# Kernel tuning notes

Hardware: AMD Instinct MI355X
Metric: run time of the kernel (lower is better)

## Reference

```python
import jax, jax.numpy as jnp
import numpy as np

B, L = 2048, 4096


def setup_inputs() -> dict:
    key = jax.random.key(0)
    k1, k2, k3 = jax.random.split(key, 3)
    j = jax.random.normal(k1, (1,), dtype=jnp.float32)
    b = jax.random.normal(k2, (2,), dtype=jnp.float32)
    observations = jax.random.randint(k3, (B, L), 0, 2, dtype=jnp.int64)
    return {"j": j, "b": b, "observations": observations}


def reference(j, b, observations):
    dt = j.dtype
    values = jnp.array([-0.5, 0.5], dtype=dt)           # 2 latent states
    pairs = values[:, None] * values[None, :]            # [2,2] outer product
    psi = j * pairs                                      # pairwise max-plus potential [2,2]
    # unary potentials: phi[b_idx, i, s] = b[obs[b_idx, i]] * values[s]
    phi = b[observations][..., None] * values            # [B, L, 2]
    zeros2 = jnp.zeros((2,), dtype=dt)

    def step(msg, phi_i):
        # max-plus message update: max over source state s of phi[s] + psi[s,t] + msg[s]
        new = jnp.max(phi_i[:, None] + psi + msg[:, None], axis=0)
        return new, new

    def per_seq(phi_seq):  # phi_seq: [L, 2]
        # forward messages: column 0 is zeros, column i+1 is msg from step i (i = 0..L-2)
        _, f = jax.lax.scan(step, zeros2, phi_seq[:-1])
        fwd = jnp.concatenate([zeros2[None], f], axis=0)       # [L, 2]
        # backward messages: iterate i = L-1 down to 1; msg from step i lands at column i-1
        _, bk = jax.lax.scan(step, zeros2, phi_seq[:0:-1])
        bwd = jnp.concatenate([bk[::-1], zeros2[None]], axis=0)  # [L, 2]
        return (phi_seq + fwd + bwd).T                          # [2, L]

    return jax.vmap(per_seq)(phi)  # [B, 2, L]
```

## Files before the change

### kernel.cpp

```cpp
#include <hip/hip_runtime.h>
#include <math.h>

#define L_SEQ 4096
#define NT 512
#define CHUNK 8
#define NW (NT/64)

struct M2 { float a00, a01, a10, a11; };

__device__ __forceinline__ M2 mpc(const M2& A, const M2& B) {
  M2 C;
  C.a00 = fmaxf(A.a00 + B.a00, A.a01 + B.a10);
  C.a01 = fmaxf(A.a00 + B.a01, A.a01 + B.a11);
  C.a10 = fmaxf(A.a10 + B.a00, A.a11 + B.a10);
  C.a11 = fmaxf(A.a10 + B.a01, A.a11 + B.a11);
  return C;
}

__device__ __forceinline__ M2 ldm(const float4& v) { return M2{v.x, v.y, v.z, v.w}; }
__device__ __forceinline__ float4 stm(const M2& m) { return make_float4(m.a00, m.a01, m.a10, m.a11); }

template <int CTRL>
__device__ __forceinline__ float dppf(float x) {
  return __int_as_float(__builtin_amdgcn_update_dpp(
      0, __float_as_int(x), CTRL, 0xf, 0xf, true));
}
template <int CTRL>
__device__ __forceinline__ M2 dpp_fetch(const M2& x) {
  M2 r;
  r.a00 = dppf<CTRL>(x.a00); r.a01 = dppf<CTRL>(x.a01);
  r.a10 = dppf<CTRL>(x.a10); r.a11 = dppf<CTRL>(x.a11);
  return r;
}

__global__ __launch_bounds__(NT, 8) void chain_fb_kernel(
    const float* __restrict__ jp, const float* __restrict__ bp,
    const int* __restrict__ obs, float* __restrict__ out) {
  __shared__ float4 T4s[16];
  __shared__ float T8a[256], T8b[256], T8c[256], T8d[256];
  __shared__ float4 wtf[NW];
  __shared__ float4 wtb[NW];

  const int t = threadIdx.x;
  const int lane = t & 63;
  const int w = t >> 6;
  const long b = blockIdx.x;

  const float P   = 0.25f * jp[0];
  const float hb0 = 0.5f * bp[0];
  const float hb1 = 0.5f * bp[1];

  const int4* rowp = (const int4*)(obs + b * L_SEQ + (long)t * CHUNK);
  int4 q0 = rowp[0], q1 = rowp[1];

  if (t < 16) {
    float u0 = (t & 1) ? hb1 : hb0;
    M2 Tt{P - u0, -u0 - P, u0 - P, u0 + P};
    #pragma unroll
    for (int k = 1; k < 4; ++k) {
      float uk = ((t >> k) & 1) ? hb1 : hb0;
      M2 Ek{P - uk, -uk - P, uk - P, uk + P};
      Tt = mpc(Tt, Ek);
    }
    T4s[t] = stm(Tt);
  }
  __syncthreads();
  if (t < 256) {
    M2 M = mpc(ldm(T4s[t & 15]), ldm(T4s[(t >> 4) & 15]));
    T8a[t] = M.a00; T8b[t] = M.a01; T8c[t] = M.a10; T8d[t] = M.a11;
  }
  const unsigned m =
      (unsigned)(q0.x & 1)       | (unsigned)(q0.y & 1) << 1 |
      (unsigned)(q0.z & 1) << 2  | (unsigned)(q0.w & 1) << 3 |
      (unsigned)(q1.x & 1) << 4  | (unsigned)(q1.y & 1) << 5 |
      (unsigned)(q1.z & 1) << 6  | (unsigned)(q1.w & 1) << 7;
  __syncthreads();

  const unsigned mrev = (unsigned)__shfl((int)m, 63 - lane);
  const unsigned r = __brev(mrev) >> 24;
  M2 T {T8a[m], T8b[m], T8c[m], T8d[m]};
  M2 Rv{T8a[r], T8b[r], T8c[r], T8d[r]};

  {
    M2 f, g;
    f = dpp_fetch<0x111>(T); g = dpp_fetch<0x111>(Rv);
    if ((lane & 15) >= 1) { T = mpc(f, T); Rv = mpc(g, Rv); }
    f = dpp_fetch<0x112>(T); g = dpp_fetch<0x112>(Rv);
    if ((lane & 15) >= 2) { T = mpc(f, T); Rv = mpc(g, Rv); }
    f = dpp_fetch<0x114>(T); g = dpp_fetch<0x114>(Rv);
    if ((lane & 15) >= 4) { T = mpc(f, T); Rv = mpc(g, Rv); }
    f = dpp_fetch<0x118>(T); g = dpp_fetch<0x118>(Rv);
    if ((lane & 15) >= 8) { T = mpc(f, T); Rv = mpc(g, Rv); }
    f = dpp_fetch<0x142>(T); g = dpp_fetch<0x142>(Rv);
    if (lane & 16)        { T = mpc(f, T); Rv = mpc(g, Rv); }
    f = dpp_fetch<0x143>(T); g = dpp_fetch<0x143>(Rv);
    if (lane >= 32)       { T = mpc(f, T); Rv = mpc(g, Rv); }
  }
  if (lane == 63) { wtf[w] = stm(T); wtb[w] = stm(Rv); }

  M2 EF{__shfl_up(T.a00, 1), __shfl_up(T.a01, 1),
        __shfl_up(T.a10, 1), __shfl_up(T.a11, 1)};
  M2 EB{__shfl_up(Rv.a00, 1), __shfl_up(Rv.a01, 1),
        __shfl_up(Rv.a10, 1), __shfl_up(Rv.a11, 1)};
  if (lane == 0) {
    EF.a00 = 0.f; EF.a01 = -INFINITY; EF.a10 = -INFINITY; EF.a11 = 0.f;
    EB.a00 = 0.f; EB.a01 = -INFINITY; EB.a10 = -INFINITY; EB.a11 = 0.f;
  }

  __syncthreads();

  M2 GF = EF, GB = EB;
  for (int ww = w - 1; ww >= 0; --ww) GF = mpc(ldm(wtf[ww]), GF);
  for (int ww = w + 1; ww < NW; ++ww) GB = mpc(ldm(wtb[ww]), GB);
  float fm0 = fmaxf(GF.a00, GF.a10), fm1 = fmaxf(GF.a01, GF.a11);
  const float bv0 = fmaxf(GB.a00, GB.a10), bv1 = fmaxf(GB.a01, GB.a11);
  float bm0 = __shfl(bv0, 63 - lane);
  float bm1 = __shfl(bv1, 63 - lane);

  float o0[CHUNK], o1[CHUNK];
  #pragma unroll
  for (int e = 0; e < CHUNK; ++e) {
    float u = ((m >> e) & 1) ? hb1 : hb0;
    float x = fm0 - u, y = fm1 + u;
    o0[e] = x; o1[e] = y;
    fm0 = fmaxf(x + P, y - P);
    fm1 = fmaxf(x - P, y + P);
  }
  #pragma unroll
  for (int e = CHUNK - 1; e >= 0; --e) {
    float u = ((m >> e) & 1) ? hb1 : hb0;
    o0[e] += bm0; o1[e] += bm1;
    float x = bm0 - u, y = bm1 + u;
    bm0 = fmaxf(x + P, y - P);
    bm1 = fmaxf(x - P, y + P);
  }

  const long base = (long)t * CHUNK;
  float* r0 = out + b * (2L * L_SEQ) + base;
  float* r1 = r0 + L_SEQ;
  ((float4*)r0)[0] = make_float4(o0[0], o0[1], o0[2], o0[3]);
  ((float4*)r0)[1] = make_float4(o0[4], o0[5], o0[6], o0[7]);
  ((float4*)r1)[0] = make_float4(o1[0], o1[1], o1[2], o1[3]);
  ((float4*)r1)[1] = make_float4(o1[4], o1[5], o1[6], o1[7]);
}

extern "C" void kernel_launch(void* const* d_in, const int* in_sizes, int n_in,
                              void* d_out, int out_size, void* d_ws, size_t ws_size,
                              hipStream_t stream) {
  const float* jp  = (const float*)d_in[0];
  const float* bp  = (const float*)d_in[1];
  const int*   obs = (const int*)d_in[2];
  float* out = (float*)d_out;
  const int B = in_sizes[2] / L_SEQ;
  chain_fb_kernel<<<B, NT, 0, stream>>>(jp, bp, obs, out);
}
```

Baseline: 24.61 us.

## Split chain scan into segment-totals and output kernels via workspace

Replaces the single 512-thread-per-sequence kernel with two launches. The first computes per-wave segment transfer matrices into a global workspace. The second recomputes the local scan, combines prefix and suffix segment totals read from global memory, and writes the outputs. This removes block-wide syncs on the combine and makes the blocks smaller, but it reads observations twice, repeats the LUT build and scan, and adds a second launch.

After: 32.47 us. 1.32x slower.

```diff
diff --git a/kernel.cpp b/kernel.cpp
--- a/kernel.cpp
+++ b/kernel.cpp
@@ -2,9 +2,10 @@
 #include <math.h>
 
 #define L_SEQ 4096
-#define NT 512
+#define SEG 512
+#define NSEG 8
+#define NT 256
 #define CHUNK 8
-#define NW (NT/64)
 
 struct M2 { float a00, a01, a10, a11; };
 
@@ -33,26 +34,9 @@
   return r;
 }
 
-__global__ __launch_bounds__(NT, 8) void chain_fb_kernel(
-    const float* __restrict__ jp, const float* __restrict__ bp,
-    const int* __restrict__ obs, float* __restrict__ out) {
-  __shared__ float4 T4s[16];
-  __shared__ float T8a[256], T8b[256], T8c[256], T8d[256];
-  __shared__ float4 wtf[NW];
-  __shared__ float4 wtb[NW];
-
-  const int t = threadIdx.x;
-  const int lane = t & 63;
-  const int w = t >> 6;
-  const long b = blockIdx.x;
-
-  const float P   = 0.25f * jp[0];
-  const float hb0 = 0.5f * bp[0];
-  const float hb1 = 0.5f * bp[1];
-
-  const int4* rowp = (const int4*)(obs + b * L_SEQ + (long)t * CHUNK);
-  int4 q0 = rowp[0], q1 = rowp[1];
-
+__device__ __forceinline__ void build_lut(
+    int t, float P, float hb0, float hb1, float4* T4s,
+    float* T8a, float* T8b, float* T8c, float* T8d) {
   if (t < 16) {
     float u0 = (t & 1) ? hb1 : hb0;
     M2 Tt{P - u0, -u0 - P, u0 - P, u0 + P};
@@ -65,38 +49,99 @@
     T4s[t] = stm(Tt);
   }
   __syncthreads();
-  if (t < 256) {
+  {
     M2 M = mpc(ldm(T4s[t & 15]), ldm(T4s[(t >> 4) & 15]));
     T8a[t] = M.a00; T8b[t] = M.a01; T8c[t] = M.a10; T8d[t] = M.a11;
   }
+  __syncthreads();
+}
+
+__device__ __forceinline__ void dpp_dual_scan(M2& T, M2& Rv, int lane) {
+  M2 f, g;
+  f = dpp_fetch<0x111>(T); g = dpp_fetch<0x111>(Rv);
+  if ((lane & 15) >= 1) { T = mpc(f, T); Rv = mpc(g, Rv); }
+  f = dpp_fetch<0x112>(T); g = dpp_fetch<0x112>(Rv);
+  if ((lane & 15) >= 2) { T = mpc(f, T); Rv = mpc(g, Rv); }
+  f = dpp_fetch<0x114>(T); g = dpp_fetch<0x114>(Rv);
+  if ((lane & 15) >= 4) { T = mpc(f, T); Rv = mpc(g, Rv); }
+  f = dpp_fetch<0x118>(T); g = dpp_fetch<0x118>(Rv);
+  if ((lane & 15) >= 8) { T = mpc(f, T); Rv = mpc(g, Rv); }
+  f = dpp_fetch<0x142>(T); g = dpp_fetch<0x142>(Rv);
+  if (lane & 16)        { T = mpc(f, T); Rv = mpc(g, Rv); }
+  f = dpp_fetch<0x143>(T); g = dpp_fetch<0x143>(Rv);
+  if (lane >= 32)       { T = mpc(f, T); Rv = mpc(g, Rv); }
+}
+
+__global__ __launch_bounds__(NT, 8) void seg_totals_kernel(
+    const float* __restrict__ jp, const float* __restrict__ bp,
+    const int* __restrict__ obs, float4* __restrict__ ws) {
+  __shared__ float4 T4s[16];
+  __shared__ float T8a[256], T8b[256], T8c[256], T8d[256];
+
+  const int t = threadIdx.x;
+  const int lane = t & 63;
+  const long g = (long)blockIdx.x * (NT / 64) + (t >> 6);
+
+  const float P   = 0.25f * jp[0];
+  const float hb0 = 0.5f * bp[0];
+  const float hb1 = 0.5f * bp[1];
+
+  const int4* rowp = (const int4*)(obs + g * SEG + lane * CHUNK);
+  int4 q0 = rowp[0], q1 = rowp[1];
+
+  build_lut(t, P, hb0, hb1, T4s, T8a, T8b, T8c, T8d);
+
   const unsigned m =
       (unsigned)(q0.x & 1)       | (unsigned)(q0.y & 1) << 1 |
       (unsigned)(q0.z & 1) << 2  | (unsigned)(q0.w & 1) << 3 |
       (unsigned)(q1.x & 1) << 4  | (unsigned)(q1.y & 1) << 5 |
       (unsigned)(q1.z & 1) << 6  | (unsigned)(q1.w & 1) << 7;
-  __syncthreads();
-
   const unsigned mrev = (unsigned)__shfl((int)m, 63 - lane);
   const unsigned r = __brev(mrev) >> 24;
   M2 T {T8a[m], T8b[m], T8c[m], T8d[m]};
   M2 Rv{T8a[r], T8b[r], T8c[r], T8d[r]};
 
-  {
-    M2 f, g;
-    f = dpp_fetch<0x111>(T); g = dpp_fetch<0x111>(Rv);
-    if ((lane & 15) >= 1) { T = mpc(f, T); Rv = mpc(g, Rv); }
-    f = dpp_fetch<0x112>(T); g = dpp_fetch<0x112>(Rv);
-    if ((lane & 15) >= 2) { T = mpc(f, T); Rv = mpc(g, Rv); }
-    f = dpp_fetch<0x114>(T); g = dpp_fetch<0x114>(Rv);
-    if ((lane & 15) >= 4) { T = mpc(f, T); Rv = mpc(g, Rv); }
-    f = dpp_fetch<0x118>(T); g = dpp_fetch<0x118>(Rv);
-    if ((lane & 15) >= 8) { T = mpc(f, T); Rv = mpc(g, Rv); }
-    f = dpp_fetch<0x142>(T); g = dpp_fetch<0x142>(Rv);
-    if (lane & 16)        { T = mpc(f, T); Rv = mpc(g, Rv); }
-    f = dpp_fetch<0x143>(T); g = dpp_fetch<0x143>(Rv);
-    if (lane >= 32)       { T = mpc(f, T); Rv = mpc(g, Rv); }
-  }
-  if (lane == 63) { wtf[w] = stm(T); wtb[w] = stm(Rv); }
+  dpp_dual_scan(T, Rv, lane);
+
+  if (lane == 63) {
+    ws[2 * g]     = stm(T);
+    ws[2 * g + 1] = stm(Rv);
+  }
+}
+
+__global__ __launch_bounds__(NT, 8) void chain_out_kernel(
+    const float* __restrict__ jp, const float* __restrict__ bp,
+    const int* __restrict__ obs, const float4* __restrict__ ws,
+    float* __restrict__ out) {
+  __shared__ float4 T4s[16];
+  __shared__ float T8a[256], T8b[256], T8c[256], T8d[256];
+
+  const int t = threadIdx.x;
+  const int lane = t & 63;
+  const long g = (long)blockIdx.x * (NT / 64) + (t >> 6);
+  const long seq = g >> 3;
+  const int  seg = (int)(g & 7);
+
+  const float P   = 0.25f * jp[0];
+  const float hb0 = 0.5f * bp[0];
+  const float hb1 = 0.5f * bp[1];
+
+  const int4* rowp = (const int4*)(obs + g * SEG + lane * CHUNK);
+  int4 q0 = rowp[0], q1 = rowp[1];
+
+  build_lut(t, P, hb0, hb1, T4s, T8a, T8b, T8c, T8d);
+
+  const unsigned m =
+      (unsigned)(q0.x & 1)       | (unsigned)(q0.y & 1) << 1 |
+      (unsigned)(q0.z & 1) << 2  | (unsigned)(q0.w & 1) << 3 |
+      (unsigned)(q1.x & 1) << 4  | (unsigned)(q1.y & 1) << 5 |
+      (unsigned)(q1.z & 1) << 6  | (unsigned)(q1.w & 1) << 7;
+  const unsigned mrev = (unsigned)__shfl((int)m, 63 - lane);
+  const unsigned r = __brev(mrev) >> 24;
+  M2 T {T8a[m], T8b[m], T8c[m], T8d[m]};
+  M2 Rv{T8a[r], T8b[r], T8c[r], T8d[r]};
+
+  dpp_dual_scan(T, Rv, lane);
 
   M2 EF{__shfl_up(T.a00, 1), __shfl_up(T.a01, 1),
         __shfl_up(T.a10, 1), __shfl_up(T.a11, 1)};
@@ -107,11 +152,10 @@
     EB.a00 = 0.f; EB.a01 = -INFINITY; EB.a10 = -INFINITY; EB.a11 = 0.f;
   }
 
-  __syncthreads();
-
   M2 GF = EF, GB = EB;
-  for (int ww = w - 1; ww >= 0; --ww) GF = mpc(ldm(wtf[ww]), GF);
-  for (int ww = w + 1; ww < NW; ++ww) GB = mpc(ldm(wtb[ww]), GB);
+  for (int s = seg - 1; s >= 0; --s) GF = mpc(ldm(ws[2 * (seq * NSEG + s)]), GF);
+  for (int s = seg + 1; s < NSEG; ++s) GB = mpc(ldm(ws[2 * (seq * NSEG + s) + 1]), GB);
+
   float fm0 = fmaxf(GF.a00, GF.a10), fm1 = fmaxf(GF.a01, GF.a11);
   const float bv0 = fmaxf(GB.a00, GB.a10), bv1 = fmaxf(GB.a01, GB.a11);
   float bm0 = __shfl(bv0, 63 - lane);
@@ -135,8 +179,8 @@
     bm1 = fmaxf(x - P, y + P);
   }
 
-  const long base = (long)t * CHUNK;
-  float* r0 = out + b * (2L * L_SEQ) + base;
+  const long base = (long)seg * SEG + lane * CHUNK;
+  float* r0 = out + seq * (2L * L_SEQ) + base;
   float* r1 = r0 + L_SEQ;
   ((float4*)r0)[0] = make_float4(o0[0], o0[1], o0[2], o0[3]);
   ((float4*)r0)[1] = make_float4(o0[4], o0[5], o0[6], o0[7]);
@@ -151,6 +195,10 @@
   const float* bp  = (const float*)d_in[1];
   const int*   obs = (const int*)d_in[2];
   float* out = (float*)d_out;
+  float4* ws = (float4*)d_ws;
   const int B = in_sizes[2] / L_SEQ;
-  chain_fb_kernel<<<B, NT, 0, stream>>>(jp, bp, obs, out);
-}
+  const int nseg_total = B * NSEG;
+  const int blocks = nseg_total / (NT / 64);
+  seg_totals_kernel<<<blocks, NT, 0, stream>>>(jp, bp, obs, ws);
+  chain_out_kernel<<<blocks, NT, 0, stream>>>(jp, bp, obs, ws, out);
+}
```

## Packed float2 max-plus math and DPP-based cross-wave prefix with vector-matrix apply

Applied to the files above, without the earlier changes.

Stores the 2x2 max-plus matrices as float2 rows so the additions can map to packed fp32 instructions on CDNA. It replaces the serial per-wave loop over earlier wave totals with a small DPP scan over the 8 wave aggregates, read out with readlane. Each lane now applies the incoming vector to its own inclusive prefix and takes the exclusive value from its neighbour through a DPP shift, where it used to carry full matrices and use shfl_up. The aim is to cut ALU and shuffle work in a latency-bound kernel, with some extra DPP steps and more subtle boundary logic as the cost.

After: 23.21 us. 5.7% less time.

```diff
diff --git a/kernel.cpp b/kernel.cpp
--- a/kernel.cpp
+++ b/kernel.cpp
@@ -6,19 +6,27 @@
 #define CHUNK 8
 #define NW (NT/64)
 
-struct M2 { float a00, a01, a10, a11; };
+typedef float f2 __attribute__((ext_vector_type(2)));
+
+__device__ __forceinline__ f2 mkf2(float a, float b) { f2 r; r.x = a; r.y = b; return r; }
+__device__ __forceinline__ f2 max2(f2 a, f2 b) { return mkf2(fmaxf(a.x, b.x), fmaxf(a.y, b.y)); }
+__device__ __forceinline__ float hmax(f2 v) { return fmaxf(v.x, v.y); }
+
+struct M2 { f2 r0, r1; };
 
 __device__ __forceinline__ M2 mpc(const M2& A, const M2& B) {
   M2 C;
-  C.a00 = fmaxf(A.a00 + B.a00, A.a01 + B.a10);
-  C.a01 = fmaxf(A.a00 + B.a01, A.a01 + B.a11);
-  C.a10 = fmaxf(A.a10 + B.a00, A.a11 + B.a10);
-  C.a11 = fmaxf(A.a10 + B.a01, A.a11 + B.a11);
+  C.r0 = max2(mkf2(A.r0.x, A.r0.x) + B.r0, mkf2(A.r0.y, A.r0.y) + B.r1);
+  C.r1 = max2(mkf2(A.r1.x, A.r1.x) + B.r0, mkf2(A.r1.y, A.r1.y) + B.r1);
   return C;
 }
+__device__ __forceinline__ f2 mapply(f2 v, const M2& M) {
+  return max2(mkf2(v.x, v.x) + M.r0, mkf2(v.y, v.y) + M.r1);
+}
+__device__ __forceinline__ f2 colmax(const M2& M) { return max2(M.r0, M.r1); }
 
-__device__ __forceinline__ M2 ldm(const float4& v) { return M2{v.x, v.y, v.z, v.w}; }
-__device__ __forceinline__ float4 stm(const M2& m) { return make_float4(m.a00, m.a01, m.a10, m.a11); }
+__device__ __forceinline__ M2 ld4(float4 v) { M2 M; M.r0 = mkf2(v.x, v.y); M.r1 = mkf2(v.z, v.w); return M; }
+__device__ __forceinline__ float4 st4(const M2& M) { return make_float4(M.r0.x, M.r0.y, M.r1.x, M.r1.y); }
 
 template <int CTRL>
 __device__ __forceinline__ float dppf(float x) {
@@ -26,20 +34,22 @@
       0, __float_as_int(x), CTRL, 0xf, 0xf, true));
 }
 template <int CTRL>
+__device__ __forceinline__ f2 dpp2(f2 x) { return mkf2(dppf<CTRL>(x.x), dppf<CTRL>(x.y)); }
+template <int CTRL>
 __device__ __forceinline__ M2 dpp_fetch(const M2& x) {
-  M2 r;
-  r.a00 = dppf<CTRL>(x.a00); r.a01 = dppf<CTRL>(x.a01);
-  r.a10 = dppf<CTRL>(x.a10); r.a11 = dppf<CTRL>(x.a11);
-  return r;
+  M2 r; r.r0 = dpp2<CTRL>(x.r0); r.r1 = dpp2<CTRL>(x.r1); return r;
+}
+__device__ __forceinline__ float rdl(float x, int l) {
+  return __int_as_float(__builtin_amdgcn_readlane(__float_as_int(x), l));
 }
 
 __global__ __launch_bounds__(NT, 8) void chain_fb_kernel(
     const float* __restrict__ jp, const float* __restrict__ bp,
     const int* __restrict__ obs, float* __restrict__ out) {
   __shared__ float4 T4s[16];
-  __shared__ float T8a[256], T8b[256], T8c[256], T8d[256];
+  __shared__ f2 T8r0[256], T8r1[256];
   __shared__ float4 wtf[NW];
-  __shared__ float4 wtb[NW];
+  __shared__ float4 wtbr[NW];
 
   const int t = threadIdx.x;
   const int lane = t & 63;
@@ -55,19 +65,19 @@
 
   if (t < 16) {
     float u0 = (t & 1) ? hb1 : hb0;
-    M2 Tt{P - u0, -u0 - P, u0 - P, u0 + P};
+    M2 Tt; Tt.r0 = mkf2(P - u0, -u0 - P); Tt.r1 = mkf2(u0 - P, u0 + P);
     #pragma unroll
     for (int k = 1; k < 4; ++k) {
       float uk = ((t >> k) & 1) ? hb1 : hb0;
-      M2 Ek{P - uk, -uk - P, uk - P, uk + P};
+      M2 Ek; Ek.r0 = mkf2(P - uk, -uk - P); Ek.r1 = mkf2(uk - P, uk + P);
       Tt = mpc(Tt, Ek);
     }
-    T4s[t] = stm(Tt);
+    T4s[t] = st4(Tt);
   }
   __syncthreads();
   if (t < 256) {
-    M2 M = mpc(ldm(T4s[t & 15]), ldm(T4s[(t >> 4) & 15]));
-    T8a[t] = M.a00; T8b[t] = M.a01; T8c[t] = M.a10; T8d[t] = M.a11;
+    M2 M = mpc(ld4(T4s[t & 15]), ld4(T4s[(t >> 4) & 15]));
+    T8r0[t] = M.r0; T8r1[t] = M.r1;
   }
   const unsigned m =
       (unsigned)(q0.x & 1)       | (unsigned)(q0.y & 1) << 1 |
@@ -78,8 +88,8 @@
 
   const unsigned mrev = (unsigned)__shfl((int)m, 63 - lane);
   const unsigned r = __brev(mrev) >> 24;
-  M2 T {T8a[m], T8b[m], T8c[m], T8d[m]};
-  M2 Rv{T8a[r], T8b[r], T8c[r], T8d[r]};
+  M2 T;  T.r0  = T8r0[m]; T.r1  = T8r1[m];
+  M2 Rv; Rv.r0 = T8r0[r]; Rv.r1 = T8r1[r];
 
   {
     M2 f, g;
@@ -96,52 +106,62 @@
     f = dpp_fetch<0x143>(T); g = dpp_fetch<0x143>(Rv);
     if (lane >= 32)       { T = mpc(f, T); Rv = mpc(g, Rv); }
   }
-  if (lane == 63) { wtf[w] = stm(T); wtb[w] = stm(Rv); }
-
-  M2 EF{__shfl_up(T.a00, 1), __shfl_up(T.a01, 1),
-        __shfl_up(T.a10, 1), __shfl_up(T.a11, 1)};
-  M2 EB{__shfl_up(Rv.a00, 1), __shfl_up(Rv.a01, 1),
-        __shfl_up(Rv.a10, 1), __shfl_up(Rv.a11, 1)};
-  if (lane == 0) {
-    EF.a00 = 0.f; EF.a01 = -INFINITY; EF.a10 = -INFINITY; EF.a11 = 0.f;
-    EB.a00 = 0.f; EB.a01 = -INFINITY; EB.a10 = -INFINITY; EB.a11 = 0.f;
-  }
+  if (lane == 63) { wtf[w] = st4(T); wtbr[7 - w] = st4(Rv); }
 
   __syncthreads();
 
-  M2 GF = EF, GB = EB;
-  for (int ww = w - 1; ww >= 0; --ww) GF = mpc(ldm(wtf[ww]), GF);
-  for (int ww = w + 1; ww < NW; ++ww) GB = mpc(ldm(wtb[ww]), GB);
-  float fm0 = fmaxf(GF.a00, GF.a10), fm1 = fmaxf(GF.a01, GF.a11);
-  const float bv0 = fmaxf(GB.a00, GB.a10), bv1 = fmaxf(GB.a01, GB.a11);
-  float bm0 = __shfl(bv0, 63 - lane);
-  float bm1 = __shfl(bv1, 63 - lane);
+  M2 Xf = ld4(wtf[lane & 7]);
+  M2 Xb = ld4(wtbr[lane & 7]);
+  {
+    M2 f, g;
+    f = dpp_fetch<0x111>(Xf); g = dpp_fetch<0x111>(Xb);
+    if ((lane & 15) >= 1) { Xf = mpc(f, Xf); Xb = mpc(g, Xb); }
+    f = dpp_fetch<0x112>(Xf); g = dpp_fetch<0x112>(Xb);
+    if ((lane & 15) >= 2) { Xf = mpc(f, Xf); Xb = mpc(g, Xb); }
+    f = dpp_fetch<0x114>(Xf); g = dpp_fetch<0x114>(Xb);
+    if ((lane & 15) >= 4) { Xf = mpc(f, Xf); Xb = mpc(g, Xb); }
+  }
+  const f2 Vf = colmax(Xf);
+  const f2 Vb = colmax(Xb);
 
-  float o0[CHUNK], o1[CHUNK];
+  f2 v, vb;
+  if (w > 0) v = mkf2(rdl(Vf.x, w - 1), rdl(Vf.y, w - 1));
+  else       v = mkf2(0.f, 0.f);
+  if (w < 7) vb = mkf2(rdl(Vb.x, 6 - w), rdl(Vb.y, 6 - w));
+  else       vb = mkf2(0.f, 0.f);
+
+  f2 wv  = mapply(v,  T);
+  f2 wvb = mapply(vb, Rv);
+  f2 fm  = dpp2<0x138>(wv);
+  f2 bmv = dpp2<0x138>(wvb);
+  if (lane == 0) { fm = v; bmv = vb; }
+  f2 bm = mkf2(__shfl(bmv.x, 63 - lane), __shfl(bmv.y, 63 - lane));
+
+  const f2 pp  = mkf2(P, -P), pm = mkf2(-P, P);
+  const f2 uvl = mkf2(-hb0, hb0), uvh = mkf2(-hb1, hb1);
+  f2 o[CHUNK];
   #pragma unroll
   for (int e = 0; e < CHUNK; ++e) {
-    float u = ((m >> e) & 1) ? hb1 : hb0;
-    float x = fm0 - u, y = fm1 + u;
-    o0[e] = x; o1[e] = y;
-    fm0 = fmaxf(x + P, y - P);
-    fm1 = fmaxf(x - P, y + P);
+    f2 uv = ((m >> e) & 1) ? uvh : uvl;
+    f2 xy = fm + uv;
+    o[e] = xy;
+    fm = mkf2(hmax(xy + pp), hmax(xy + pm));
   }
   #pragma unroll
   for (int e = CHUNK - 1; e >= 0; --e) {
-    float u = ((m >> e) & 1) ? hb1 : hb0;
-    o0[e] += bm0; o1[e] += bm1;
-    float x = bm0 - u, y = bm1 + u;
-    bm0 = fmaxf(x + P, y - P);
-    bm1 = fmaxf(x - P, y + P);
+    f2 uv = ((m >> e) & 1) ? uvh : uvl;
+    o[e] += bm;
+    f2 xy = bm + uv;
+    bm = mkf2(hmax(xy + pp), hmax(xy + pm));
   }
 
   const long base = (long)t * CHUNK;
   float* r0 = out + b * (2L * L_SEQ) + base;
   float* r1 = r0 + L_SEQ;
-  ((float4*)r0)[0] = make_float4(o0[0], o0[1], o0[2], o0[3]);
-  ((float4*)r0)[1] = make_float4(o0[4], o0[5], o0[6], o0[7]);
-  ((float4*)r1)[0] = make_float4(o1[0], o1[1], o1[2], o1[3]);
-  ((float4*)r1)[1] = make_float4(o1[4], o1[5], o1[6], o1[7]);
+  ((float4*)r0)[0] = make_float4(o[0].x, o[1].x, o[2].x, o[3].x);
+  ((float4*)r0)[1] = make_float4(o[4].x, o[5].x, o[6].x, o[7].x);
+  ((float4*)r1)[0] = make_float4(o[0].y, o[1].y, o[2].y, o[3].y);
+  ((float4*)r1)[1] = make_float4(o[4].y, o[5].y, o[6].y, o[7].y);
 }
 
 extern "C" void kernel_launch(void* const* d_in, const int* in_sizes, int n_in,
```
